# Optimization experiments

Hardware: AMD Instinct MI355X
Metric: run time of the kernel (lower is better)

The kernel has to match this reference:

```python
import jax, jax.numpy as jnp
import numpy as np

B, S, DMAX, NMEL, DM, K = 8, 100, 12, 80, 128, 9
T = S * DMAX  # 1200 max mel frames
EPS = 1e-5  # BatchNorm eps (eval mode, running_mean=0, running_var=1)


def setup_inputs() -> dict:
    key = jax.random.key(0)
    ks = jax.random.split(key, 16)
    durations = jax.random.randint(ks[0], (B, S), 4, DMAX + 1).astype(jnp.int32)
    mel_len = jnp.sum(durations, axis=1).astype(jnp.int32)
    src_len = jnp.full((B,), S, dtype=jnp.int32)
    mel = jax.random.normal(ks[1], (B, T, NMEL), dtype=jnp.float32)
    # conv stack params (xavier-ish uniform)
    s1 = float(np.sqrt(6.0 / (1 * K + DM * K)))
    w1 = jax.random.uniform(ks[2], (DM, 1, 1, K), minval=-s1, maxval=s1, dtype=jnp.float32)
    g1 = 1.0 + 0.1 * jax.random.normal(ks[3], (DM,), dtype=jnp.float32)
    be1 = 0.1 * jax.random.normal(ks[4], (DM,), dtype=jnp.float32)
    s2 = float(np.sqrt(6.0 / (DM * K + 1 * K)))
    w2 = jax.random.uniform(ks[5], (1, DM, 1, K), minval=-s2, maxval=s2, dtype=jnp.float32)
    g2 = 1.0 + 0.1 * jax.random.normal(ks[6], (1,), dtype=jnp.float32)
    be2 = 0.1 * jax.random.normal(ks[7], (1,), dtype=jnp.float32)
    # BiGRU params (pytorch layout: gates [r|z|n] stacked -> 3*H rows)
    sh = float(1.0 / np.sqrt(DM))
    u = lambda k, shape: jax.random.uniform(k, shape, minval=-sh, maxval=sh, dtype=jnp.float32)
    w_ih_f = u(ks[8], (3 * DM, NMEL)); w_hh_f = u(ks[9], (3 * DM, DM))
    b_ih_f = u(ks[10], (3 * DM,));    b_hh_f = u(ks[11], (3 * DM,))
    w_ih_b = u(ks[12], (3 * DM, NMEL)); w_hh_b = u(ks[13], (3 * DM, DM))
    b_ih_b = u(ks[14], (3 * DM,));    b_hh_b = u(ks[15], (3 * DM,))
    return {"mel": mel, "durations": durations, "mel_len": mel_len, "src_len": src_len,
            "w1": w1, "g1": g1, "be1": be1, "w2": w2, "g2": g2, "be2": be2,
            "w_ih_f": w_ih_f, "w_hh_f": w_hh_f, "b_ih_f": b_ih_f, "b_hh_f": b_hh_f,
            "w_ih_b": w_ih_b, "w_hh_b": w_hh_b, "b_ih_b": b_ih_b, "b_hh_b": b_hh_b}


def _bn_eval(x, g, b):
    # eval-mode BatchNorm2d with running_mean=0, running_var=1; x [B,C,T,M]
    scale = g / jnp.sqrt(1.0 + EPS)
    return x * scale[None, :, None, None] + b[None, :, None, None]


def _gru_scan(xs_seq, reset_seq, w_hh, b_hh):
    # xs_seq [T,B,3H] precomputed input projections; reset_seq [T,B] 1.0 -> reset h to 0
    H = w_hh.shape[1]
    Bn = xs_seq.shape[1]

    def step(h, inp):
        xg, rst = inp
        h = h * (1.0 - rst)[:, None]
        hg = h @ w_hh.T + b_hh
        xr, xz, xn = jnp.split(xg, 3, axis=-1)
        hr, hz, hn = jnp.split(hg, 3, axis=-1)
        r = jax.nn.sigmoid(xr + hr)
        z = jax.nn.sigmoid(xz + hz)
        n = jnp.tanh(xn + r * hn)
        h_new = (1.0 - z) * n + z * h
        return h_new, h_new

    h0 = jnp.zeros((Bn, H), xs_seq.dtype)
    _, hs = jax.lax.scan(step, h0, (xs_seq, reset_seq))
    return hs  # [T,B,H]


def reference(mel, durations, mel_len, src_len, w1, g1, be1, w2, g2, be2,
              w_ih_f, w_hh_f, b_ih_f, b_hh_f, w_ih_b, w_hh_b, b_ih_b, b_hh_b):
    pad = (K - 1) // 2
    # conv stack: kernel (1,K) mixes only the mel-channel axis -> apply to full mel once
    x = mel[:, None, :, :]  # [B,1,T,M]
    x = jax.lax.conv_general_dilated(x, w1, (1, 1), [(0, 0), (pad, pad)])
    x = jax.nn.relu(_bn_eval(x, g1, be1))
    x = jax.lax.conv_general_dilated(x, w2, (1, 1), [(0, 0), (pad, pad)])
    x = jax.nn.relu(_bn_eval(x, g2, be2))
    x = x[:, 0]  # [B,T,M]

    # segment boundaries from durations (all phones valid here, durations > 0)
    cum = jnp.cumsum(durations, axis=1)      # [B,S]
    starts = cum - durations                 # segment start frame per phone
    ends = cum - 1                           # segment end frame per phone
    bidx = jnp.arange(B)[:, None]
    start_mask = jnp.zeros((B, T), x.dtype).at[bidx, starts].set(1.0)
    end_mask = jnp.zeros((B, T), x.dtype).at[bidx, ends].set(1.0)

    # forward direction: reset h at segment starts, read h at segment ends
    xf = jnp.einsum('btm,gm->tbg', x, w_ih_f) + b_ih_f
    Hf = _gru_scan(xf, start_mask.T, w_hh_f, b_hh_f)           # [T,B,H]
    # backward direction: scan reversed time, reset at original segment ends
    xb = jnp.einsum('btm,gm->tbg', x, w_ih_b) + b_ih_b
    Hb = _gru_scan(xb[::-1], end_mask.T[::-1], w_hh_b, b_hh_b)[::-1]  # [T,B,H], orig time

    hf = jnp.take_along_axis(jnp.transpose(Hf, (1, 0, 2)), ends[..., None], axis=1)    # [B,S,H]
    hb = jnp.take_along_axis(jnp.transpose(Hb, (1, 0, 2)), starts[..., None], axis=1)  # [B,S,H]
    out = jnp.concatenate([hf, hb], axis=-1)  # [B,S,2H]
    valid = (jnp.arange(S)[None, :] < src_len[:, None])[..., None]
    return jnp.where(valid, out, 0.0)
```

## Files before the change

kernel.cpp:

```cpp
#include <hip/hip_runtime.h>
#include <math.h>

#define BB   8
#define SS   100
#define TT   1200
#define NM   80
#define DMC  128
#define KK   9
#define G3   384
#define NROW (BB*TT)

typedef __attribute__((ext_vector_type(8))) short short8;
typedef __attribute__((ext_vector_type(4))) float f32x4;
typedef __attribute__((ext_vector_type(2))) float f32x2;

__device__ __forceinline__ float sigmoid_(float v) { return 1.f / (1.f + __expf(-v)); }
__device__ __forceinline__ float tanh_(float v) {
    float a = fabsf(v);
    float e = __expf(-2.f * a);
    float t = (1.f - e) / (1.f + e);
    return copysignf(t, v);
}
__device__ __forceinline__ unsigned short f2bf(float f) {
    unsigned int u = __float_as_uint(f);
    unsigned int r = (u + 0x7fffu + ((u >> 16) & 1u)) >> 16;
    return (unsigned short)r;
}
__device__ __forceinline__ f32x2 pk_fma(f32x2 a, f32x2 b, f32x2 c) {
    f32x2 d;
    asm("v_pk_fma_f32 %0, %1, %2, %3" : "=v"(d) : "v"(a), "v"(b), "v"(c));
    return d;
}

__global__ __launch_bounds__(1024) void k_prep(
    const float* __restrict__ whf, const float* __restrict__ whb,
    const float* __restrict__ wif, const float* __restrict__ wib,
    const float* __restrict__ bf, const float* __restrict__ bbv,
    const int* __restrict__ dur,
    unsigned short* __restrict__ wph, unsigned short* __restrict__ wpl,
    unsigned short* __restrict__ wih_h, unsigned short* __restrict__ wih_l,
    float* __restrict__ biasc, int* __restrict__ starts) {
    int blk = blockIdx.x;
    int tid = threadIdx.x;
    if (blk < 12) {
        int idx = blk * 1024 + tid;
        int lane = idx & 63;
        int k32  = (idx >> 6) & 3;
        int tau  = (idx >> 8) % 24;
        int dir  = idx / (24 * 4 * 64);
        const float* w = dir ? whb : whf;
        int g = tau * 16 + (lane & 15);
        int kbase = k32 * 32 + (lane >> 4) * 8;
#pragma unroll
        for (int j = 0; j < 8; j++) {
            float v = w[g * DMC + kbase + j];
            unsigned short hi = f2bf(v);
            float hif = __uint_as_float(((unsigned)hi) << 16);
            unsigned short lo = f2bf(v - hif);
            wph[idx * 8 + j] = hi;
            wpl[idx * 8 + j] = lo;
        }
    } else if (blk < 21) {
        int idx = (blk - 12) * 1024 + tid;
        int lane = idx & 63;
        int ks   = (idx >> 6) % 3;
        int tau  = idx / (3 * 64);
        int gate = tau * 16 + (lane & 15);
        int kb   = ks * 32 + (lane >> 4) * 8;
        const float* w = (gate < G3) ? (wif + gate * NM) : (wib + (gate - G3) * NM);
#pragma unroll
        for (int j = 0; j < 8; j++) {
            int k = kb + j;
            float v = (k < NM) ? w[k] : 0.f;
            unsigned short hi = f2bf(v);
            float hif = __uint_as_float(((unsigned)hi) << 16);
            unsigned short lo = f2bf(v - hif);
            wih_h[idx * 8 + j] = hi;
            wih_l[idx * 8 + j] = lo;
        }
    } else {
        __shared__ int buf[BB][128];
        int s = tid & 127, b = tid >> 7;
        int v = (s < SS) ? dur[b * SS + s] : 0;
        buf[b][s] = v;
        __syncthreads();
        for (int off = 1; off < 128; off <<= 1) {
            int t = (s >= off) ? buf[b][s - off] : 0;
            __syncthreads();
            buf[b][s] += t;
            __syncthreads();
        }
        if (s < SS) starts[b * SS + s] = buf[b][s] - v;
        if (tid < 768) biasc[tid] = (tid < G3) ? bf[tid] : bbv[tid - G3];
    }
}

__global__ __launch_bounds__(256) void k_conv(
    const float* __restrict__ mel, const int* __restrict__ mel_len,
    const float* __restrict__ w1, const float* __restrict__ g1, const float* __restrict__ be1,
    const float* __restrict__ w2, const float* __restrict__ g2, const float* __restrict__ be2,
    float* __restrict__ xout) {
    int b  = blockIdx.y;
    int t0 = blockIdx.x * 2;
    int ml = mel_len[b];
    if (t0 >= ml) return;

    __shared__ __align__(16) f32x2 mp2[96];
    __shared__ __align__(16) f32x2 part2[8][82];

    int tid = threadIdx.x;
    int mq = tid >> 6, g = tid & 63;
    int ms = 20 * mq;
    const float inv_sqrt = 0.9999950000374997f;

    if (tid < 192) {
        int rr = tid / 96, i = tid - rr * 96;
        float v = 0.f;
        if (i >= 8 && i < 88) v = mel[(b * TT + t0 + rr) * NM + i - 8];
        ((float*)mp2)[i * 2 + rr] = v;
    }
    __syncthreads();

    f32x2 c[20];
#pragma unroll
    for (int m = 0; m < 20; m++) c[m] = (f32x2){0.f, 0.f};

#pragma unroll 1
    for (int dd = 0; dd < 2; dd++) {
        int d = g + 64 * dd;
        float sc = g1[d] * inv_sqrt;
        f32x2 w1p[KK], w2p[KK];
#pragma unroll
        for (int k = 0; k < KK; k++) {
            float a = w1[d * KK + k] * sc;
            float bq = w2[d * KK + k];
            w1p[k] = (f32x2){a, a};
            w2p[k] = (f32x2){bq, bq};
        }
        float sb = be1[d];

        f32x2 mw[12];
        {
            const float4* p4 = (const float4*)(mp2 + ms);
#pragma unroll
            for (int q = 0; q < 6; q++) {
                float4 v = p4[q];
                mw[2 * q]     = (f32x2){v.x, v.y};
                mw[2 * q + 1] = (f32x2){v.z, v.w};
            }
        }
#pragma unroll
        for (int ch = 0; ch < 7; ch++) {
#pragma unroll
            for (int jj = 0; jj < 4; jj++) {
                int off = ch * 4 + jj;
                f32x2 yv = (f32x2){sb, sb};
#pragma unroll
                for (int k = 0; k < KK; k++) yv = pk_fma(w1p[k], mw[jj + k], yv);
                yv[0] = fmaxf(yv[0], 0.f);
                yv[1] = fmaxf(yv[1], 0.f);
                int j = ms + off;
                if (j < 4 || j >= 84) yv = (f32x2){0.f, 0.f};
#pragma unroll
                for (int k = 0; k < KK; k++) {
                    int mo = off - k;
                    if (mo >= 0 && mo < 20) c[mo] = pk_fma(w2p[k], yv, c[mo]);
                }
            }
            if (ch < 6) {
#pragma unroll
                for (int q = 0; q < 8; q++) mw[q] = mw[q + 4];
                const float4* p4 = (const float4*)(mp2 + ms + ch * 4 + 12);
                float4 a0 = p4[0], a1 = p4[1];
                mw[8]  = (f32x2){a0.x, a0.y};
                mw[9]  = (f32x2){a0.z, a0.w};
                mw[10] = (f32x2){a1.x, a1.y};
                mw[11] = (f32x2){a1.z, a1.w};
            }
        }
    }

#pragma unroll
    for (int m = 0; m < 20; m++) {
        c[m][0] += __shfl_xor(c[m][0], 1);
        c[m][1] += __shfl_xor(c[m][1], 1);
        c[m][0] += __shfl_xor(c[m][0], 2);
        c[m][1] += __shfl_xor(c[m][1], 2);
        c[m][0] += __shfl_xor(c[m][0], 4);
        c[m][1] += __shfl_xor(c[m][1], 4);
    }
    if ((g & 7) == 0) {
        int p = g >> 3;
#pragma unroll
        for (int m = 0; m < 20; m++) part2[p][ms + m] = c[m];
    }
    __syncthreads();

    if (tid < 160) {
        int rr = (tid >= 80) ? 1 : 0;
        int m  = tid - 80 * rr;
        int t  = t0 + rr;
        if (t < ml) {
            float s = 0.f;
#pragma unroll
            for (int p = 0; p < 8; p++) s += part2[p][m][rr];
            float v = fmaxf(0.f, fmaf(s, g2[0] * inv_sqrt, be2[0]));
            xout[(b * TT + t) * NM + m] = v;
        }
    }
}

__global__ __launch_bounds__(512, 2) void k_gru(
    const float* __restrict__ x,
    const unsigned short* __restrict__ wph, const unsigned short* __restrict__ wpl,
    const unsigned short* __restrict__ wih_h, const unsigned short* __restrict__ wih_l,
    const float* __restrict__ biasc,
    const int* __restrict__ dur_all, const int* __restrict__ starts,
    const int* __restrict__ src_len,
    const float* __restrict__ bhf, const float* __restrict__ bhb,
    float* __restrict__ out) {
    int sblk = blockIdx.x;
    int b    = blockIdx.y;
    int dir  = blockIdx.z;
    int s0 = sblk * 16;

    __shared__ __align__(16) short8 xbh[12][192];
    __shared__ __align__(16) short8 xbl[12][192];
    __shared__ __align__(16) unsigned short hbh[2][2048];
    __shared__ __align__(16) unsigned short hbl[2][2048];
    __shared__ int sdur[16], sstart[16];

    int tid  = threadIdx.x;
    int wave = tid >> 6, lane = tid & 63;
    int quad = lane >> 4, seg = lane & 15;

    if (tid < 16) {
        int ss = s0 + tid;
        sdur[tid]   = (ss < SS) ? dur_all[b * SS + ss] : 0;
        sstart[tid] = (ss < SS) ? starts[b * SS + ss]  : 0;
    }
    for (int i = tid; i < 2048; i += 512) { hbh[0][i] = 0; hbl[0][i] = 0; }

    short8 Ah[3][4], Al[3][4];
    const short8* wph8 = (const short8*)wph;
    const short8* wpl8 = (const short8*)wpl;
#pragma unroll
    for (int tt = 0; tt < 3; tt++)
#pragma unroll
        for (int k32 = 0; k32 < 4; k32++) {
            int idx = ((dir * 24 + wave + 8 * tt) * 4 + k32) * 64 + lane;
            Ah[tt][k32] = wph8[idx];
            Al[tt][k32] = wpl8[idx];
        }
    short8 Gh[3][3], Gl[3][3];
    const short8* wih_h8 = (const short8*)wih_h;
    const short8* wih_l8 = (const short8*)wih_l;
#pragma unroll
    for (int tt = 0; tt < 3; tt++)
#pragma unroll
        for (int ks = 0; ks < 3; ks++) {
            int idx = ((dir * 24 + wave + 8 * tt) * 3 + ks) * 64 + lane;
            Gh[tt][ks] = wih_h8[idx];
            Gl[tt][ks] = wih_l8[idx];
        }

    int s = s0 + seg;
    int sd = (s < SS) ? dur_all[b * SS + s] : 0;
    int slb = src_len[b];
    const float* bih = biasc + dir * G3;
    const float* bhh = dir ? bhb : bhf;
    int j0 = wave * 16 + quad * 4;
    float4 i_r = *(const float4*)&bih[j0];
    float4 i_z = *(const float4*)&bih[DMC + j0];
    float4 bxn = *(const float4*)&bih[2 * DMC + j0];
    float4 h_r = *(const float4*)&bhh[j0];
    float4 h_z = *(const float4*)&bhh[DMC + j0];
    float4 bhn = *(const float4*)&bhh[2 * DMC + j0];
    float4 br = make_float4(i_r.x + h_r.x, i_r.y + h_r.y, i_r.z + h_r.z, i_r.w + h_r.w);
    float4 bz = make_float4(i_z.x + h_z.x, i_z.y + h_z.y, i_z.z + h_z.z, i_z.w + h_z.w);
    float4 h = make_float4(0.f, 0.f, 0.f, 0.f);

    int idx8 = (j0 >> 5) * 64 + ((j0 >> 3) & 3) * 16 + seg;
    int wbase = idx8 * 8 + (j0 & 7);

    __syncthreads();

#pragma unroll
    for (int q = 0; q < 5; q++) {
        int u = tid + q * 512;
        if (u < 12 * 192) {
            int it  = u / 192;
            int rem = u - it * 192;
            int ks = rem >> 6, ln = rem & 63;
            int sg = ln & 15, qq = ln >> 4;
            int kb = ks * 32 + qq * 8;
            short8 hi8 = {0,0,0,0,0,0,0,0}, lo8 = {0,0,0,0,0,0,0,0};
            int d2 = sdur[sg];
            if (kb < NM && it < d2) {
                int t = dir ? (sstart[sg] + d2 - 1 - it) : (sstart[sg] + it);
                const float* xr = x + (size_t)(b * TT + t) * NM + kb;
#pragma unroll
                for (int j = 0; j < 8; j++) {
                    float v = xr[j];
                    unsigned short hi = f2bf(v);
                    hi8[j] = (short)hi;
                    lo8[j] = (short)f2bf(v - __uint_as_float(((unsigned)hi) << 16));
                }
            }
            xbh[it][rem] = hi8;
            xbl[it][rem] = lo8;
        }
    }
    __syncthreads();

    for (int i = 0; i < 12; i++) {
        int p = i & 1;
        bool act = (i < sd);

        f32x4 axr = (f32x4){0.f,0.f,0.f,0.f};
        f32x4 axz = (f32x4){0.f,0.f,0.f,0.f};
        f32x4 axn = (f32x4){0.f,0.f,0.f,0.f};
        f32x4 ahr = (f32x4){0.f,0.f,0.f,0.f};
        f32x4 ahz = (f32x4){0.f,0.f,0.f,0.f};
        f32x4 ahn = (f32x4){0.f,0.f,0.f,0.f};
#pragma unroll
        for (int ks = 0; ks < 3; ks++) {
            short8 Bxh = xbh[i][ks * 64 + lane];
            short8 Bxl = xbl[i][ks * 64 + lane];
            axr = __builtin_amdgcn_mfma_f32_16x16x32_bf16(Gh[0][ks], Bxh, axr, 0, 0, 0);
            axr = __builtin_amdgcn_mfma_f32_16x16x32_bf16(Gh[0][ks], Bxl, axr, 0, 0, 0);
            axr = __builtin_amdgcn_mfma_f32_16x16x32_bf16(Gl[0][ks], Bxh, axr, 0, 0, 0);
            axz = __builtin_amdgcn_mfma_f32_16x16x32_bf16(Gh[1][ks], Bxh, axz, 0, 0, 0);
            axz = __builtin_amdgcn_mfma_f32_16x16x32_bf16(Gh[1][ks], Bxl, axz, 0, 0, 0);
            axz = __builtin_amdgcn_mfma_f32_16x16x32_bf16(Gl[1][ks], Bxh, axz, 0, 0, 0);
            axn = __builtin_amdgcn_mfma_f32_16x16x32_bf16(Gh[2][ks], Bxh, axn, 0, 0, 0);
            axn = __builtin_amdgcn_mfma_f32_16x16x32_bf16(Gh[2][ks], Bxl, axn, 0, 0, 0);
            axn = __builtin_amdgcn_mfma_f32_16x16x32_bf16(Gl[2][ks], Bxh, axn, 0, 0, 0);
        }
#pragma unroll
        for (int k32 = 0; k32 < 4; k32++) {
            short8 Bh = ((const short8*)hbh[p])[k32 * 64 + lane];
            short8 Bl = ((const short8*)hbl[p])[k32 * 64 + lane];
            ahr = __builtin_amdgcn_mfma_f32_16x16x32_bf16(Ah[0][k32], Bh, ahr, 0, 0, 0);
            ahr = __builtin_amdgcn_mfma_f32_16x16x32_bf16(Ah[0][k32], Bl, ahr, 0, 0, 0);
            ahr = __builtin_amdgcn_mfma_f32_16x16x32_bf16(Al[0][k32], Bh, ahr, 0, 0, 0);
            ahz = __builtin_amdgcn_mfma_f32_16x16x32_bf16(Ah[1][k32], Bh, ahz, 0, 0, 0);
            ahz = __builtin_amdgcn_mfma_f32_16x16x32_bf16(Ah[1][k32], Bl, ahz, 0, 0, 0);
            ahz = __builtin_amdgcn_mfma_f32_16x16x32_bf16(Al[1][k32], Bh, ahz, 0, 0, 0);
            ahn = __builtin_amdgcn_mfma_f32_16x16x32_bf16(Ah[2][k32], Bh, ahn, 0, 0, 0);
            ahn = __builtin_amdgcn_mfma_f32_16x16x32_bf16(Ah[2][k32], Bl, ahn, 0, 0, 0);
            ahn = __builtin_amdgcn_mfma_f32_16x16x32_bf16(Al[2][k32], Bh, ahn, 0, 0, 0);
        }

        if (act) {
            float hv[4]  = {h.x, h.y, h.z, h.w};
            float brv[4] = {br.x, br.y, br.z, br.w};
            float bzv[4] = {bz.x, bz.y, bz.z, bz.w};
            float bxv[4] = {bxn.x, bxn.y, bxn.z, bxn.w};
            float bhv[4] = {bhn.x, bhn.y, bhn.z, bhn.w};
#pragma unroll
            for (int cmp = 0; cmp < 4; cmp++) {
                float r = sigmoid_(axr[cmp] + ahr[cmp] + brv[cmp]);
                float z = sigmoid_(axz[cmp] + ahz[cmp] + bzv[cmp]);
                float n = tanh_(axn[cmp] + bxv[cmp] + r * (ahn[cmp] + bhv[cmp]));
                hv[cmp] = (1.f - z) * n + z * hv[cmp];
            }
            h = make_float4(hv[0], hv[1], hv[2], hv[3]);
            if (i == sd - 1) {
                float4 vout = (s < slb) ? h : make_float4(0.f, 0.f, 0.f, 0.f);
                *(float4*)&out[(b * SS + s) * (2 * DMC) + dir * DMC + j0] = vout;
            }
        }

        {
            float hv[4] = {h.x, h.y, h.z, h.w};
            unsigned short hs_[4], ls_[4];
#pragma unroll
            for (int cmp = 0; cmp < 4; cmp++) {
                unsigned short hi = f2bf(hv[cmp]);
                float hif = __uint_as_float(((unsigned)hi) << 16);
                hs_[cmp] = hi;
                ls_[cmp] = f2bf(hv[cmp] - hif);
            }
            *(ushort4*)&hbh[1 - p][wbase] = make_ushort4(hs_[0], hs_[1], hs_[2], hs_[3]);
            *(ushort4*)&hbl[1 - p][wbase] = make_ushort4(ls_[0], ls_[1], ls_[2], ls_[3]);
        }
        __syncthreads();
    }
}

extern "C" void kernel_launch(void* const* d_in, const int* in_sizes, int n_in,
                              void* d_out, int out_size, void* d_ws, size_t ws_size,
                              hipStream_t stream) {
    const float* mel      = (const float*)d_in[0];
    const int*   durations= (const int*)  d_in[1];
    const int*   mel_len  = (const int*)  d_in[2];
    const int*   src_len  = (const int*)  d_in[3];
    const float* w1       = (const float*)d_in[4];
    const float* g1       = (const float*)d_in[5];
    const float* be1      = (const float*)d_in[6];
    const float* w2       = (const float*)d_in[7];
    const float* g2       = (const float*)d_in[8];
    const float* be2      = (const float*)d_in[9];
    const float* w_ih_f   = (const float*)d_in[10];
    const float* w_hh_f   = (const float*)d_in[11];
    const float* b_ih_f   = (const float*)d_in[12];
    const float* b_hh_f   = (const float*)d_in[13];
    const float* w_ih_b   = (const float*)d_in[14];
    const float* w_hh_b   = (const float*)d_in[15];
    const float* b_ih_b   = (const float*)d_in[16];
    const float* b_hh_b   = (const float*)d_in[17];
    float* out = (float*)d_out;

    float* x    = (float*)d_ws;
    unsigned short* wph   = (unsigned short*)(x + NROW * NM);
    unsigned short* wpl   = wph + 2 * 24 * 4 * 64 * 8;
    unsigned short* wih_h = wpl + 2 * 24 * 4 * 64 * 8;
    unsigned short* wih_l = wih_h + 48 * 3 * 64 * 8;
    float* biasc = (float*)(wih_l + 48 * 3 * 64 * 8);
    int*   starts= (int*)(biasc + 768);

    k_prep<<<22, 1024, 0, stream>>>(w_hh_f, w_hh_b, w_ih_f, w_ih_b, b_ih_f, b_ih_b,
                                    durations, wph, wpl, wih_h, wih_l, biasc, starts);
    k_conv<<<dim3(TT / 2, BB), 256, 0, stream>>>(mel, mel_len, w1, g1, be1, w2, g2, be2, x);
    k_gru<<<dim3(7, 8, 2), 512, 0, stream>>>(x, wph, wpl, wih_h, wih_l, biasc,
                                             durations, starts, src_len,
                                             b_hh_f, b_hh_b, out);
}
```

Measured before the change: 166.5 us.

## Fuse weight-prep into conv kernel and stage conv weights in shared memory

Merges the separate weight-packing/prefix-sum prep kernel into the conv kernel as extra blocks, removing one launch and its serialization gap. The prefix sum becomes a wave-shuffle scan. Conv blocks now cooperatively load the BN-scaled w1 and w2 into LDS before use, and edge masking uses packed multiplies by keep factors instead of index checks. Every conv block now reloads about 2.3K weights into LDS, which adds per-block global traffic and LDS footprint.

```diff
diff --git a/kernel.cpp b/kernel.cpp
--- a/kernel.cpp
+++ b/kernel.cpp
@@ -31,8 +31,17 @@
     asm("v_pk_fma_f32 %0, %1, %2, %3" : "=v"(d) : "v"(a), "v"(b), "v"(c));
     return d;
 }
-
-__global__ __launch_bounds__(1024) void k_prep(
+__device__ __forceinline__ f32x2 pk_mul(f32x2 a, f32x2 b) {
+    f32x2 d;
+    asm("v_pk_mul_f32 %0, %1, %2" : "=v"(d) : "v"(a), "v"(b));
+    return d;
+}
+
+__global__ __launch_bounds__(256) void k_convprep(
+    const float* __restrict__ mel, const int* __restrict__ mel_len,
+    const float* __restrict__ w1, const float* __restrict__ g1, const float* __restrict__ be1,
+    const float* __restrict__ w2, const float* __restrict__ g2, const float* __restrict__ be2,
+    float* __restrict__ xout,
     const float* __restrict__ whf, const float* __restrict__ whb,
     const float* __restrict__ wif, const float* __restrict__ wib,
     const float* __restrict__ bf, const float* __restrict__ bbv,
@@ -40,75 +49,83 @@
     unsigned short* __restrict__ wph, unsigned short* __restrict__ wpl,
     unsigned short* __restrict__ wih_h, unsigned short* __restrict__ wih_l,
     float* __restrict__ biasc, int* __restrict__ starts) {
-    int blk = blockIdx.x;
+    int bx = blockIdx.x;
+    int b  = blockIdx.y;
     int tid = threadIdx.x;
-    if (blk < 12) {
-        int idx = blk * 1024 + tid;
-        int lane = idx & 63;
-        int k32  = (idx >> 6) & 3;
-        int tau  = (idx >> 8) % 24;
-        int dir  = idx / (24 * 4 * 64);
-        const float* w = dir ? whb : whf;
-        int g = tau * 16 + (lane & 15);
-        int kbase = k32 * 32 + (lane >> 4) * 8;
-#pragma unroll
-        for (int j = 0; j < 8; j++) {
-            float v = w[g * DMC + kbase + j];
-            unsigned short hi = f2bf(v);
-            float hif = __uint_as_float(((unsigned)hi) << 16);
-            unsigned short lo = f2bf(v - hif);
-            wph[idx * 8 + j] = hi;
-            wpl[idx * 8 + j] = lo;
-        }
-    } else if (blk < 21) {
-        int idx = (blk - 12) * 1024 + tid;
-        int lane = idx & 63;
-        int ks   = (idx >> 6) % 3;
-        int tau  = idx / (3 * 64);
-        int gate = tau * 16 + (lane & 15);
-        int kb   = ks * 32 + (lane >> 4) * 8;
-        const float* w = (gate < G3) ? (wif + gate * NM) : (wib + (gate - G3) * NM);
-#pragma unroll
-        for (int j = 0; j < 8; j++) {
-            int k = kb + j;
-            float v = (k < NM) ? w[k] : 0.f;
-            unsigned short hi = f2bf(v);
-            float hif = __uint_as_float(((unsigned)hi) << 16);
-            unsigned short lo = f2bf(v - hif);
-            wih_h[idx * 8 + j] = hi;
-            wih_l[idx * 8 + j] = lo;
-        }
-    } else {
-        __shared__ int buf[BB][128];
-        int s = tid & 127, b = tid >> 7;
-        int v = (s < SS) ? dur[b * SS + s] : 0;
-        buf[b][s] = v;
-        __syncthreads();
-        for (int off = 1; off < 128; off <<= 1) {
-            int t = (s >= off) ? buf[b][s - off] : 0;
-            __syncthreads();
-            buf[b][s] += t;
-            __syncthreads();
-        }
-        if (s < SS) starts[b * SS + s] = buf[b][s] - v;
-        if (tid < 768) biasc[tid] = (tid < G3) ? bf[tid] : bbv[tid - G3];
-    }
-}
-
-__global__ __launch_bounds__(256) void k_conv(
-    const float* __restrict__ mel, const int* __restrict__ mel_len,
-    const float* __restrict__ w1, const float* __restrict__ g1, const float* __restrict__ be1,
-    const float* __restrict__ w2, const float* __restrict__ g2, const float* __restrict__ be2,
-    float* __restrict__ xout) {
-    int b  = blockIdx.y;
-    int t0 = blockIdx.x * 2;
+
+    if (bx >= 600) {
+        int pid = (bx - 600) * 8 + b;
+        if (pid < 87) {
+            int u = pid * 256 + tid;
+            if (u < 12288) {
+                int idx = u;
+                int lane = idx & 63;
+                int k32  = (idx >> 6) & 3;
+                int tau  = (idx >> 8) % 24;
+                int dir  = idx / (24 * 4 * 64);
+                const float* w = dir ? whb : whf;
+                int gg = tau * 16 + (lane & 15);
+                int kbase = k32 * 32 + (lane >> 4) * 8;
+#pragma unroll
+                for (int j = 0; j < 8; j++) {
+                    float v = w[gg * DMC + kbase + j];
+                    unsigned short hi = f2bf(v);
+                    float hif = __uint_as_float(((unsigned)hi) << 16);
+                    unsigned short lo = f2bf(v - hif);
+                    wph[idx * 8 + j] = hi;
+                    wpl[idx * 8 + j] = lo;
+                }
+            } else if (u < 21504) {
+                int idx = u - 12288;
+                int lane = idx & 63;
+                int ks   = (idx >> 6) % 3;
+                int tau  = idx / (3 * 64);
+                int gate = tau * 16 + (lane & 15);
+                int kb   = ks * 32 + (lane >> 4) * 8;
+                const float* w = (gate < G3) ? (wif + gate * NM) : (wib + (gate - G3) * NM);
+#pragma unroll
+                for (int j = 0; j < 8; j++) {
+                    int k = kb + j;
+                    float v = (k < NM) ? w[k] : 0.f;
+                    unsigned short hi = f2bf(v);
+                    float hif = __uint_as_float(((unsigned)hi) << 16);
+                    unsigned short lo = f2bf(v - hif);
+                    wih_h[idx * 8 + j] = hi;
+                    wih_l[idx * 8 + j] = lo;
+                }
+            } else {
+                int v = u - 21504;
+                biasc[v] = (v < G3) ? bf[v] : bbv[v - G3];
+            }
+        } else {
+            int batch = tid >> 5, l = tid & 31;
+            int run = 0;
+#pragma unroll
+            for (int c = 0; c < 4; c++) {
+                int s = c * 32 + l;
+                int v = (s < SS) ? dur[batch * SS + s] : 0;
+                int xv = v;
+#pragma unroll
+                for (int off = 1; off < 32; off <<= 1) {
+                    int t = __shfl_up(xv, off, 32);
+                    if (l >= off) xv += t;
+                }
+                if (s < SS) starts[batch * SS + s] = run + xv - v;
+                run += __shfl(xv, 31, 32);
+            }
+        }
+        return;
+    }
+
+    int t0 = bx * 2;
     int ml = mel_len[b];
     if (t0 >= ml) return;
 
     __shared__ __align__(16) f32x2 mp2[96];
     __shared__ __align__(16) f32x2 part2[8][82];
-
-    int tid = threadIdx.x;
+    __shared__ float w1s[DMC * KK];
+    __shared__ float w2s[DMC * KK];
+
     int mq = tid >> 6, g = tid & 63;
     int ms = 20 * mq;
     const float inv_sqrt = 0.9999950000374997f;
@@ -119,25 +136,34 @@
         if (i >= 8 && i < 88) v = mel[(b * TT + t0 + rr) * NM + i - 8];
         ((float*)mp2)[i * 2 + rr] = v;
     }
+    for (int u = tid; u < DMC * KK; u += 256) {
+        w1s[u] = w1[u] * (g1[u / KK] * inv_sqrt);
+        w2s[u] = w2[u];
+    }
     __syncthreads();
 
     f32x2 c[20];
 #pragma unroll
     for (int m = 0; m < 20; m++) c[m] = (f32x2){0.f, 0.f};
+
+    float klf = (mq == 0) ? 0.f : 1.f;
+    float khf = (mq == 3) ? 0.f : 1.f;
+    f32x2 keeplo = (f32x2){klf, klf};
+    f32x2 keephi = (f32x2){khf, khf};
 
 #pragma unroll 1
     for (int dd = 0; dd < 2; dd++) {
         int d = g + 64 * dd;
-        float sc = g1[d] * inv_sqrt;
         f32x2 w1p[KK], w2p[KK];
 #pragma unroll
         for (int k = 0; k < KK; k++) {
-            float a = w1[d * KK + k] * sc;
-            float bq = w2[d * KK + k];
+            float a  = w1s[d * KK + k];
+            float bq = w2s[d * KK + k];
             w1p[k] = (f32x2){a, a};
             w2p[k] = (f32x2){bq, bq};
         }
         float sb = be1[d];
+        f32x2 sbp = (f32x2){sb, sb};
 
         f32x2 mw[12];
         {
@@ -151,20 +177,26 @@
         }
 #pragma unroll
         for (int ch = 0; ch < 7; ch++) {
+            f32x2 yv4[4];
 #pragma unroll
             for (int jj = 0; jj < 4; jj++) {
                 int off = ch * 4 + jj;
-                f32x2 yv = (f32x2){sb, sb};
+                f32x2 yv = sbp;
 #pragma unroll
                 for (int k = 0; k < KK; k++) yv = pk_fma(w1p[k], mw[jj + k], yv);
                 yv[0] = fmaxf(yv[0], 0.f);
                 yv[1] = fmaxf(yv[1], 0.f);
-                int j = ms + off;
-                if (j < 4 || j >= 84) yv = (f32x2){0.f, 0.f};
+                if (off < 4)   yv = pk_mul(yv, keeplo);
+                if (off >= 24) yv = pk_mul(yv, keephi);
+                yv4[jj] = yv;
+            }
+#pragma unroll
+            for (int jj = 0; jj < 4; jj++) {
+                int off = ch * 4 + jj;
 #pragma unroll
                 for (int k = 0; k < KK; k++) {
                     int mo = off - k;
-                    if (mo >= 0 && mo < 20) c[mo] = pk_fma(w2p[k], yv, c[mo]);
+                    if (mo >= 0 && mo < 20) c[mo] = pk_fma(w2p[k], yv4[jj], c[mo]);
                 }
             }
             if (ch < 6) {
@@ -420,9 +452,10 @@
     float* biasc = (float*)(wih_l + 48 * 3 * 64 * 8);
     int*   starts= (int*)(biasc + 768);
 
-    k_prep<<<22, 1024, 0, stream>>>(w_hh_f, w_hh_b, w_ih_f, w_ih_b, b_ih_f, b_ih_b,
-                                    durations, wph, wpl, wih_h, wih_l, biasc, starts);
-    k_conv<<<dim3(TT / 2, BB), 256, 0, stream>>>(mel, mel_len, w1, g1, be1, w2, g2, be2, x);
+    k_convprep<<<dim3(611, BB), 256, 0, stream>>>(
+        mel, mel_len, w1, g1, be1, w2, g2, be2, x,
+        w_hh_f, w_hh_b, w_ih_f, w_ih_b, b_ih_f, b_ih_b,
+        durations, wph, wpl, wih_h, wih_l, biasc, starts);
     k_gru<<<dim3(7, 8, 2), 512, 0, stream>>>(x, wph, wpl, wih_h, wih_l, biasc,
                                              durations, starts, src_len,
                                              b_hh_f, b_hh_b, out);
```

New measurement: 160.8 us. -3.4%, faster.
